# Performance work log

Measured on AMD Instinct MI355X. Metric: run time of the kernel, lower is better.

Reference implementation:

```python
import jax, jax.numpy as jnp
import numpy as np

B, N, E = 256, 128, 262144
LABEL_DIM, MAX_DEGREE, RW_DIM = 29, 16, 16
F = 128
NUM_LABELS = LABEL_DIM + MAX_DEGREE + RW_DIM  # 61
SK_ITER, SK_TAU = 6, 1.0


def _edges(k):
    k1, k2, k3 = jax.random.split(k, 3)
    g = jax.random.randint(k1, (E,), 0, B)
    src = g * N + jax.random.randint(k2, (E,), 0, N)
    dst = g * N + jax.random.randint(k3, (E,), 0, N)
    return src, dst


def setup_inputs():
    key = jax.random.key(0)
    ks = jax.random.split(key, 20)
    ntot = B * N
    s = 0.05
    nrm = lambda k, shp: jax.random.normal(k, shp, dtype=jnp.float32) * s
    src1, dst1 = _edges(ks[3])
    src2, dst2 = _edges(ks[7])
    return {
        'x1': jax.random.uniform(ks[0], (ntot, LABEL_DIM), dtype=jnp.float32),
        'cent1': jax.random.randint(ks[1], (ntot,), 0, MAX_DEGREE),
        'rw1': jax.random.uniform(ks[2], (ntot, RW_DIM), dtype=jnp.float32),
        'src1': src1, 'dst1': dst1,
        'x2': jax.random.uniform(ks[4], (ntot, LABEL_DIM), dtype=jnp.float32),
        'cent2': jax.random.randint(ks[5], (ntot,), 0, MAX_DEGREE),
        'rw2': jax.random.uniform(ks[6], (ntot, RW_DIM), dtype=jnp.float32),
        'src2': src2, 'dst2': dst2,
        'degree_emb': nrm(ks[8], (MAX_DEGREE, MAX_DEGREE)),
        'init_W': nrm(ks[9], (NUM_LABELS, F)), 'init_b': jnp.zeros((F,), jnp.float32),
        'W1': nrm(ks[10], (F, F)), 'b1': jnp.zeros((F,), jnp.float32),
        'W2': nrm(ks[11], (F, F)), 'b2': jnp.zeros((F,), jnp.float32),
        'W3': nrm(ks[12], (F, F)), 'b3': jnp.zeros((F,), jnp.float32),
        'A_aff': nrm(ks[13], (F, F)) + jnp.eye(F, dtype=jnp.float32),
        'sc_W1': nrm(ks[14], (8 * F, 64)), 'sc_b1': jnp.zeros((64,), jnp.float32),
        'sc_W2': nrm(ks[15], (64, 1)), 'sc_b2': jnp.zeros((1,), jnp.float32),
        'topk': 8,
    }


def gcn_conv(x, W, b, src, dst):
    # GCNConv: x' = D^{-1/2} (A + I) D^{-1/2} x W + b
    n = x.shape[0]
    h = x @ W
    loops = jnp.arange(n)
    s = jnp.concatenate([src, loops])
    d = jnp.concatenate([dst, loops])
    deg = jax.ops.segment_sum(jnp.ones_like(d, dtype=h.dtype), d, n)
    dinv = jax.lax.rsqrt(jnp.maximum(deg, 1.0))
    w = dinv[s] * dinv[d]
    return jax.ops.segment_sum(h[s] * w[:, None], d, n) + b


def conv_pass(feat, src, dst, W1, b1, W2, b2, W3, b3):
    f1 = gcn_conv(feat, W1, b1, src, dst)
    f2 = gcn_conv(jax.nn.relu(f1), W2, b2, src, dst)
    f3 = gcn_conv(jax.nn.relu(f2), W3, b3, src, dst)
    return f1, f2, f3


def affinity(xa, xb, A):
    Xa = xa.reshape(B, N, -1)
    Xb = xb.reshape(B, N, -1)
    return jnp.einsum('bif,fg,bjg->bij', Xa, A, Xb)


def soft_topk(scores, ks_tgt, n_iter, tau):
    # Entropic-OT soft top-k (Xie et al.) over flattened affinity entries vs 2 anchors,
    # normalized by SK_ITER log-domain Sinkhorn iterations.
    b, n, m = scores.shape
    L = n * m
    x = scores.reshape(b, L)
    a_lo = x.min(axis=1, keepdims=True) - 1.0
    a_hi = x.max(axis=1, keepdims=True) + 1.0
    anchors = jnp.concatenate([a_lo, a_hi], axis=1)      # [b, 2]
    logK = -jnp.abs(x[:, :, None] - anchors[:, None, :]) / tau  # [b, L, 2]
    log_mu = jnp.full((b, L), -jnp.log(float(L)), dtype=x.dtype)
    k = ks_tgt[:, None]
    nu = jnp.concatenate([(L - k) / L, k / L], axis=1)   # [b, 2]
    log_nu = jnp.log(nu)

    def body(carry, _):
        f, g = carry
        f = log_mu - jax.nn.logsumexp(logK + g[:, None, :], axis=2)
        g = log_nu - jax.nn.logsumexp(logK + f[:, :, None], axis=1)
        return (f, g), None

    init = (jnp.zeros((b, L), x.dtype), jnp.zeros((b, 2), x.dtype))
    (f, g), _ = jax.lax.scan(body, init, None, length=n_iter)
    gamma = jnp.exp(logK + f[:, :, None] + g[:, None, :])
    prob = (gamma[:, :, 1] * L).reshape(b, n, m)
    return gamma, prob


def reference(x1, cent1, rw1, src1, dst1, x2, cent2, rw2, src2, dst2,
              degree_emb, init_W, init_b, W1, b1, W2, b2, W3, b3, A_aff,
              sc_W1, sc_b1, sc_W2, sc_b2, topk):
    feat1 = jax.nn.relu(jnp.concatenate([x1, degree_emb[cent1], rw1], axis=1) @ init_W + init_b)
    feat2 = jax.nn.relu(jnp.concatenate([x2, degree_emb[cent2], rw2], axis=1) @ init_W + init_b)
    f11, f12, f13 = conv_pass(feat1, src1, dst1, W1, b1, W2, b2, W3, b3)
    f21, f22, f23 = conv_pass(feat2, src2, dst2, W1, b1, W2, b2, W3, b3)

    gt_ks = jnp.full((B,), topk / 2.0, dtype=feat1.dtype)
    _, sim1 = soft_topk(affinity(feat1, feat2, A_aff), gt_ks, SK_ITER, SK_TAU)
    _, sim2 = soft_topk(affinity(f13, f23, A_aff), gt_ks, SK_ITER, SK_TAU)

    gf1 = jnp.concatenate([feat1, f11, f12, f13], axis=1).reshape(B, N, -1).sum(axis=1)   # global_add_pool
    gf2 = jnp.concatenate([feat2, f21, f22, f23], axis=1).reshape(B, N, -1).max(axis=1)   # global_max_pool
    scores = jnp.concatenate([gf1, gf2], axis=1)  # [B, 8F]
    h = jax.nn.relu(scores @ sc_W1 + sc_b1)
    ged = jax.nn.sigmoid((h @ sc_W2 + sc_b2).reshape(-1))
    return ged, sim1, sim2
```

## Files before the change

### kernel.cpp

```cpp
#include <hip/hip_runtime.h>
#include <math.h>

#define BATCH 256
#define NNODE 128
#define NT    32768
#define FDIM  128
#define NEDGE 262144
#define LBL   29
#define MAXDEG 16
#define RWD   16
#define NTF   (NT * FDIM)
#define ESTRIDE 2048

__global__ void k_deg2(const int* __restrict__ dst1, const int* __restrict__ dst2,
                       int* __restrict__ d1, int* __restrict__ d2) {
  int e = blockIdx.x * 256 + threadIdx.x;
  if (e < NEDGE) atomicAdd(&d1[dst1[e]], 1);
  else if (e < 2 * NEDGE) atomicAdd(&d2[dst2[e - NEDGE]], 1);
}
__global__ __launch_bounds__(128) void k_scanl(const int* __restrict__ degi1,
                                               int* __restrict__ ofs1, int* __restrict__ cur1,
                                               float* __restrict__ dinv1,
                                               const int* __restrict__ degi2,
                                               int* __restrict__ ofs2, int* __restrict__ cur2,
                                               float* __restrict__ dinv2) {
  const int side = blockIdx.x >> 8;
  const int g = blockIdx.x & 255;
  const int* degi = side ? degi2 : degi1;
  int* ofs   = side ? ofs2  : ofs1;
  int* cur   = side ? cur2  : cur1;
  float* dnv = side ? dinv2 : dinv1;
  const int t = threadIdx.x;
  const int node = g * NNODE + t;
  int dg = degi[node];
  dnv[node] = rsqrtf((float)(dg + 1));
  int lane = t & 63, wv = t >> 6;
  int v = dg;
  for (int off = 1; off < 64; off <<= 1) {
    int u = __shfl_up(v, off);
    if (lane >= off) v += u;
  }
  __shared__ int wsum[2];
  if (lane == 63) wsum[wv] = v;
  __syncthreads();
  int excl = v - dg + (wv ? wsum[0] : 0);
  int base = g * ESTRIDE + excl;
  ofs[node] = base;
  cur[node] = base;
}
__global__ void k_fill2(const int* __restrict__ src1, const int* __restrict__ dst1,
                        int* __restrict__ cur1, int* __restrict__ csr1,
                        const int* __restrict__ src2, const int* __restrict__ dst2,
                        int* __restrict__ cur2, int* __restrict__ csr2) {
  int e = blockIdx.x * 256 + threadIdx.x;
  if (e < NEDGE) {
    int pos = atomicAdd(&cur1[dst1[e]], 1);
    csr1[pos] = src1[e];
  } else if (e < 2 * NEDGE) {
    e -= NEDGE;
    int pos = atomicAdd(&cur2[dst2[e]], 1);
    csr2[pos] = src2[e];
  }
}

__global__ __launch_bounds__(256, 2) void k_chain(
    const float* __restrict__ x1, const int* __restrict__ cent1, const float* __restrict__ rw1,
    const float* __restrict__ x2, const int* __restrict__ cent2, const float* __restrict__ rw2,
    const float* __restrict__ demb,
    const float* __restrict__ initW, const float* __restrict__ initb,
    const float* __restrict__ W1, const float* __restrict__ b1,
    const float* __restrict__ W2, const float* __restrict__ b2,
    const float* __restrict__ W3, const float* __restrict__ b3,
    const int* __restrict__ ofs1, const int* __restrict__ end1, const int* __restrict__ csr1,
    const int* __restrict__ ofs2, const int* __restrict__ end2, const int* __restrict__ csr2,
    const float* __restrict__ dinv1, const float* __restrict__ dinv2,
    float* __restrict__ feat1G, float* __restrict__ feat2G,
    float* __restrict__ f13G, float* __restrict__ f23G,
    float* __restrict__ gfs) {
  __shared__ float X[128 * 132];
  __shared__ float WcB[16 * 132];
  __shared__ float dvL[128];
  __shared__ float bL[128];
  __shared__ int   oL[128], enL[128];

  const int t = threadIdx.x;
  const int side = blockIdx.x >> 8;
  const int g = blockIdx.x & 255;
  const int nb = g * NNODE;

  const float* xg    = side ? x2 : x1;
  const int*   centg = side ? cent2 : cent1;
  const float* rwg   = side ? rw2 : rw1;
  const int*   ofsg  = side ? ofs2 : ofs1;
  const int*   endg  = side ? end2 : end1;
  const int*   csrg  = side ? csr2 : csr1;
  const float* dinvg = side ? dinv2 : dinv1;
  float* featG = side ? feat2G : feat1G;
  float* f3G   = side ? f23G : f13G;

  const int e_base = ofsg[nb];
  if (t < 128) {
    dvL[t] = dinvg[nb + t];
    oL[t]  = ofsg[nb + t] - e_base;
    enL[t] = endg[nb + t] - e_base;
  }
  {
    int d = t >> 1, sub = t & 1;
    int node = nb + d;
    int ct = centg[node];
    const float* xr = xg + (size_t)node * LBL;
    const float* er = demb + ct * MAXDEG;
    const float* rr = rwg + (size_t)node * RWD;
    for (int c = sub * 34; c < sub * 34 + 34; ++c) {
      float v = 0.f;
      if (c < LBL) v = xr[c];
      else if (c < LBL + MAXDEG) v = er[c - LBL];
      else if (c < 61) v = rr[c - 45];
      X[d * 68 + c] = v;
    }
  }
  __syncthreads();

  const int rg = t >> 3;
  const int jq = (t & 7) * 4;

  {
    float acc[4][16] = {};
    for (int kc = 0; kc < 64; kc += 16) {
      __syncthreads();
#pragma unroll
      for (int u = 0; u < 2; ++u) {
        int ll = t + 256 * u;
        int row = ll >> 5, c4 = (ll & 31) * 4;
        int gk = kc + row;
        float4 w = (gk < 61) ? *reinterpret_cast<const float4*>(&initW[(size_t)gk * FDIM + c4])
                             : make_float4(0.f, 0.f, 0.f, 0.f);
        *reinterpret_cast<float4*>(&WcB[row * 132 + c4]) = w;
      }
      if (kc == 0 && t < 128) bL[t] = initb[t];
      __syncthreads();
      for (int kk = 0; kk < 16; kk += 4) {
        float av[4][4];
#pragma unroll
        for (int r = 0; r < 4; ++r) {
          float4 tmp = *reinterpret_cast<const float4*>(&X[(rg + 32 * r) * 68 + kc + kk]);
          av[r][0] = tmp.x; av[r][1] = tmp.y; av[r][2] = tmp.z; av[r][3] = tmp.w;
        }
#pragma unroll
        for (int c = 0; c < 4; ++c) {
          float4 w0 = *reinterpret_cast<const float4*>(&WcB[(kk + c) * 132 + jq]);
          float4 w1 = *reinterpret_cast<const float4*>(&WcB[(kk + c) * 132 + 32 + jq]);
          float4 w2 = *reinterpret_cast<const float4*>(&WcB[(kk + c) * 132 + 64 + jq]);
          float4 w3 = *reinterpret_cast<const float4*>(&WcB[(kk + c) * 132 + 96 + jq]);
#pragma unroll
          for (int r = 0; r < 4; ++r) {
            float a = av[r][c];
            acc[r][0]  += a * w0.x; acc[r][1]  += a * w0.y; acc[r][2]  += a * w0.z; acc[r][3]  += a * w0.w;
            acc[r][4]  += a * w1.x; acc[r][5]  += a * w1.y; acc[r][6]  += a * w1.z; acc[r][7]  += a * w1.w;
            acc[r][8]  += a * w2.x; acc[r][9]  += a * w2.y; acc[r][10] += a * w2.z; acc[r][11] += a * w2.w;
            acc[r][12] += a * w3.x; acc[r][13] += a * w3.y; acc[r][14] += a * w3.z; acc[r][15] += a * w3.w;
          }
        }
      }
    }
    __syncthreads();
#pragma unroll
    for (int r = 0; r < 4; ++r) {
      int row = rg + 32 * r;
#pragma unroll
      for (int q = 0; q < 4; ++q) {
        int col = q * 32 + jq;
        float4 bl = *reinterpret_cast<const float4*>(&bL[col]);
        float4 o = make_float4(fmaxf(acc[r][q * 4 + 0] + bl.x, 0.f),
                               fmaxf(acc[r][q * 4 + 1] + bl.y, 0.f),
                               fmaxf(acc[r][q * 4 + 2] + bl.z, 0.f),
                               fmaxf(acc[r][q * 4 + 3] + bl.w, 0.f));
        *reinterpret_cast<float4*>(&X[row * 132 + col]) = o;
        *reinterpret_cast<float4*>(&featG[(size_t)(nb + row) * FDIM + col]) = o;
      }
    }
    __syncthreads();
  }

#define POOL_LAYER(layer)                                                            \
  {                                                                                  \
    int j4 = (t & 31) * 4, qq = t >> 5;                                              \
    float4 pv = side ? make_float4(-INFINITY, -INFINITY, -INFINITY, -INFINITY)       \
                     : make_float4(0.f, 0.f, 0.f, 0.f);                              \
    for (int r = 0; r < 16; ++r) {                                                   \
      float4 fv = *reinterpret_cast<const float4*>(&X[(qq * 16 + r) * 132 + j4]);    \
      if (side) { pv.x = fmaxf(pv.x, fv.x); pv.y = fmaxf(pv.y, fv.y);                \
                  pv.z = fmaxf(pv.z, fv.z); pv.w = fmaxf(pv.w, fv.w); }              \
      else      { pv.x += fv.x; pv.y += fv.y; pv.z += fv.z; pv.w += fv.w; }          \
    }                                                                                \
    *reinterpret_cast<float4*>(&WcB[qq * 128 + j4]) = pv;                            \
    __syncthreads();                                                                 \
    if (t < 128) {                                                                   \
      float v = side ? -INFINITY : 0.f;                                              \
      for (int q2 = 0; q2 < 8; ++q2) {                                               \
        float w2 = WcB[q2 * 128 + t];                                                \
        v = side ? fmaxf(v, w2) : (v + w2);                                          \
      }                                                                              \
      gfs[g * 1024 + side * 512 + (layer) * 128 + t] = v;                            \
    }                                                                                \
  }

  POOL_LAYER(0)

  for (int l = 0; l < 3; ++l) {
    const float* Wg = (l == 0) ? W1 : (l == 1) ? W2 : W3;
    const float* bg = (l == 0) ? b1 : (l == 1) ? b2 : b3;
    float acc[4][16] = {};
    for (int kc = 0; kc < 128; kc += 16) {
      __syncthreads();
#pragma unroll
      for (int u = 0; u < 2; ++u) {
        int ll = t + 256 * u;
        int row = ll >> 5, c4 = (ll & 31) * 4;
        *reinterpret_cast<float4*>(&WcB[row * 132 + c4]) =
            *reinterpret_cast<const float4*>(&Wg[(size_t)(kc + row) * FDIM + c4]);
      }
      if (kc == 0 && t < 128) bL[t] = bg[t];
      __syncthreads();
      for (int kk = 0; kk < 16; kk += 4) {
        float av[4][4];
#pragma unroll
        for (int r = 0; r < 4; ++r) {
          float4 tmp = *reinterpret_cast<const float4*>(&X[(rg + 32 * r) * 132 + kc + kk]);
          if (l > 0) {
            tmp.x = fmaxf(tmp.x, 0.f); tmp.y = fmaxf(tmp.y, 0.f);
            tmp.z = fmaxf(tmp.z, 0.f); tmp.w = fmaxf(tmp.w, 0.f);
          }
          av[r][0] = tmp.x; av[r][1] = tmp.y; av[r][2] = tmp.z; av[r][3] = tmp.w;
        }
#pragma unroll
        for (int c = 0; c < 4; ++c) {
          float4 w0 = *reinterpret_cast<const float4*>(&WcB[(kk + c) * 132 + jq]);
          float4 w1 = *reinterpret_cast<const float4*>(&WcB[(kk + c) * 132 + 32 + jq]);
          float4 w2 = *reinterpret_cast<const float4*>(&WcB[(kk + c) * 132 + 64 + jq]);
          float4 w3 = *reinterpret_cast<const float4*>(&WcB[(kk + c) * 132 + 96 + jq]);
#pragma unroll
          for (int r = 0; r < 4; ++r) {
            float a = av[r][c];
            acc[r][0]  += a * w0.x; acc[r][1]  += a * w0.y; acc[r][2]  += a * w0.z; acc[r][3]  += a * w0.w;
            acc[r][4]  += a * w1.x; acc[r][5]  += a * w1.y; acc[r][6]  += a * w1.z; acc[r][7]  += a * w1.w;
            acc[r][8]  += a * w2.x; acc[r][9]  += a * w2.y; acc[r][10] += a * w2.z; acc[r][11] += a * w2.w;
            acc[r][12] += a * w3.x; acc[r][13] += a * w3.y; acc[r][14] += a * w3.z; acc[r][15] += a * w3.w;
          }
        }
      }
    }
    __syncthreads();
#pragma unroll
    for (int r = 0; r < 4; ++r) {
      int row = rg + 32 * r;
#pragma unroll
      for (int q = 0; q < 4; ++q) {
        int col = q * 32 + jq;
        *reinterpret_cast<float4*>(&X[row * 132 + col]) =
            make_float4(acc[r][q * 4 + 0], acc[r][q * 4 + 1],
                        acc[r][q * 4 + 2], acc[r][q * 4 + 3]);
      }
    }
    __syncthreads();

    {
      int d = t >> 1, fc = (t & 1) * 64;
      float dd = dvL[d];
      float4 a[16];
#pragma unroll
      for (int u = 0; u < 16; ++u) {
        float4 hv = *reinterpret_cast<const float4*>(&X[d * 132 + fc + u * 4]);
        a[u] = make_float4(dd * hv.x, dd * hv.y, dd * hv.z, dd * hv.w);
      }
      int o0 = oL[d], o1 = enL[d];
      int sj = (o0 < o1) ? (csrg[e_base + o0] - nb) : 0;
      for (int j = o0; j < o1; ++j) {
        int sn = (j + 1 < o1) ? (csrg[e_base + j + 1] - nb) : 0;
        float w = dvL[sj];
#pragma unroll
        for (int u = 0; u < 16; ++u) {
          float4 hv = *reinterpret_cast<const float4*>(&X[sj * 132 + fc + u * 4]);
          a[u].x += w * hv.x; a[u].y += w * hv.y; a[u].z += w * hv.z; a[u].w += w * hv.w;
        }
        sj = sn;
      }
      __syncthreads();
#pragma unroll
      for (int u = 0; u < 16; ++u) {
        float4 bl = *reinterpret_cast<const float4*>(&bL[fc + u * 4]);
        float4 o = make_float4(bl.x + dd * a[u].x, bl.y + dd * a[u].y,
                               bl.z + dd * a[u].z, bl.w + dd * a[u].w);
        *reinterpret_cast<float4*>(&X[d * 132 + fc + u * 4]) = o;
        if (l == 2)
          *reinterpret_cast<float4*>(&f3G[(size_t)(nb + d) * FDIM + fc + u * 4]) = o;
      }
    }
    __syncthreads();

    POOL_LAYER(l + 1)
  }
#undef POOL_LAYER
}

__global__ __launch_bounds__(1024) void k_sim(const float* __restrict__ F1s1,
                                              const float* __restrict__ F2s1,
                                              const float* __restrict__ F1s2,
                                              const float* __restrict__ F2s2,
                                              const float* __restrict__ Aaff,
                                              const int* __restrict__ topk,
                                              float* __restrict__ S1,
                                              float* __restrict__ S2) {
  __shared__ float X1[128 * 132];
  __shared__ float X2[128 * 132];
  __shared__ float rA[16], rB[16], bc[2];

  const int t = threadIdx.x;
  const int half = blockIdx.x >> 8;
  const int b = blockIdx.x & 255;
  const float* F1b = (half ? F1s2 : F1s1) + (size_t)b * NNODE * FDIM;
  const float* F2b = (half ? F2s2 : F2s1) + (size_t)b * NNODE * FDIM;
  float* Sout = (half ? S2 : S1) + (size_t)b * NNODE * NNODE;

#pragma unroll
  for (int p = 0; p < 4; ++p) {
    int fi = t + 1024 * p;
    int row = fi >> 5, c4 = (fi & 31) * 4;
    *reinterpret_cast<float4*>(&X1[row * 132 + c4]) =
        *reinterpret_cast<const float4*>(&Aaff[(size_t)row * FDIM + c4]);
  }
  {
    int row = t >> 3;
    int cq  = (t & 7) * 4;
#pragma unroll
    for (int p = 0; p < 4; ++p) {
      int c4 = p * 32 + cq;
      float4 v = *reinterpret_cast<const float4*>(&F2b[(size_t)row * FDIM + c4]);
      X2[(c4 + 0) * 132 + row] = v.x;
      X2[(c4 + 1) * 132 + row] = v.y;
      X2[(c4 + 2) * 132 + row] = v.z;
      X2[(c4 + 3) * 132 + row] = v.w;
    }
  }
  __syncthreads();

  const int rw = t >> 4;
  const int jq4 = (t & 15) * 4;
  const float* f1r0 = F1b + (size_t)rw * FDIM;
  const float* f1r1 = F1b + (size_t)(rw + 64) * FDIM;

  float acc[2][8] = {};

  for (int k0 = 0; k0 < 128; k0 += 4) {
    float4 a40 = *reinterpret_cast<const float4*>(&f1r0[k0]);
    float4 a41 = *reinterpret_cast<const float4*>(&f1r1[k0]);
    float av0[4] = {a40.x, a40.y, a40.z, a40.w};
    float av1[4] = {a41.x, a41.y, a41.z, a41.w};
#pragma unroll
    for (int c = 0; c < 4; ++c) {
      const float* wb = &X1[(k0 + c) * 132];
      float4 w0 = *reinterpret_cast<const float4*>(&wb[jq4]);
      float4 w1 = *reinterpret_cast<const float4*>(&wb[jq4 + 64]);
      float a0 = av0[c], a1 = av1[c];
      acc[0][0] += a0 * w0.x; acc[0][1] += a0 * w0.y; acc[0][2] += a0 * w0.z; acc[0][3] += a0 * w0.w;
      acc[0][4] += a0 * w1.x; acc[0][5] += a0 * w1.y; acc[0][6] += a0 * w1.z; acc[0][7] += a0 * w1.w;
      acc[1][0] += a1 * w0.x; acc[1][1] += a1 * w0.y; acc[1][2] += a1 * w0.z; acc[1][3] += a1 * w0.w;
      acc[1][4] += a1 * w1.x; acc[1][5] += a1 * w1.y; acc[1][6] += a1 * w1.z; acc[1][7] += a1 * w1.w;
    }
  }
  __syncthreads();
  *reinterpret_cast<float4*>(&X1[rw * 132 + jq4]) =
      make_float4(acc[0][0], acc[0][1], acc[0][2], acc[0][3]);
  *reinterpret_cast<float4*>(&X1[rw * 132 + jq4 + 64]) =
      make_float4(acc[0][4], acc[0][5], acc[0][6], acc[0][7]);
  *reinterpret_cast<float4*>(&X1[(rw + 64) * 132 + jq4]) =
      make_float4(acc[1][0], acc[1][1], acc[1][2], acc[1][3]);
  *reinterpret_cast<float4*>(&X1[(rw + 64) * 132 + jq4 + 64]) =
      make_float4(acc[1][4], acc[1][5], acc[1][6], acc[1][7]);

#pragma unroll
  for (int r = 0; r < 2; ++r)
#pragma unroll
    for (int j = 0; j < 8; ++j) acc[r][j] = 0.f;
  __syncthreads();

  for (int k0 = 0; k0 < 128; k0 += 4) {
    float4 a40 = *reinterpret_cast<const float4*>(&X1[rw * 132 + k0]);
    float4 a41 = *reinterpret_cast<const float4*>(&X1[(rw + 64) * 132 + k0]);
    float av0[4] = {a40.x, a40.y, a40.z, a40.w};
    float av1[4] = {a41.x, a41.y, a41.z, a41.w};
#pragma unroll
    for (int c = 0; c < 4; ++c) {
      const float* wb = &X2[(k0 + c) * 132];
      float4 w0 = *reinterpret_cast<const float4*>(&wb[jq4]);
      float4 w1 = *reinterpret_cast<const float4*>(&wb[jq4 + 64]);
      float a0 = av0[c], a1 = av1[c];
      acc[0][0] += a0 * w0.x; acc[0][1] += a0 * w0.y; acc[0][2] += a0 * w0.z; acc[0][3] += a0 * w0.w;
      acc[0][4] += a0 * w1.x; acc[0][5] += a0 * w1.y; acc[0][6] += a0 * w1.z; acc[0][7] += a0 * w1.w;
      acc[1][0] += a1 * w0.x; acc[1][1] += a1 * w0.y; acc[1][2] += a1 * w0.z; acc[1][3] += a1 * w0.w;
      acc[1][4] += a1 * w1.x; acc[1][5] += a1 * w1.y; acc[1][6] += a1 * w1.z; acc[1][7] += a1 * w1.w;
    }
  }

  const float* af = &acc[0][0];
  const int wave = t >> 6, lane = t & 63;
  {
    float mn = af[0], mx = af[0];
#pragma unroll
    for (int u = 1; u < 16; ++u) { mn = fminf(mn, af[u]); mx = fmaxf(mx, af[u]); }
    for (int off = 32; off; off >>= 1) {
      mn = fminf(mn, __shfl_down(mn, off));
      mx = fmaxf(mx, __shfl_down(mx, off));
    }
    if (lane == 0) { rA[wave] = mn; rB[wave] = mx; }
    __syncthreads();
    if (t < 16) {
      mn = rA[t]; mx = rB[t];
      for (int off = 8; off; off >>= 1) {
        mn = fminf(mn, __shfl_down(mn, off));
        mx = fmaxf(mx, __shfl_down(mx, off));
      }
      if (t == 0) { bc[0] = mn - 1.f; bc[1] = mx + 1.f; }
    }
    __syncthreads();
  }
  float a_lo = bc[0], a_hi = bc[1];

  float p[16], q[16];
#pragma unroll
  for (int u = 0; u < 16; ++u) {
    p[u] = __expf(a_lo - af[u]);
    q[u] = __expf(af[u] - a_hi);
  }

  const float Lf = (float)(NNODE * NNODE);
  float kt = 0.5f * (float)topk[0];

  float E0 = 1.f, E1 = 1.f, E0p = 1.f, E1p = 1.f;
  for (int it = 0; it < 6; ++it) {
    E0p = E0; E1p = E1;
    float r0 = 0.f, r1 = 0.f;
#pragma unroll
    for (int u = 0; u < 16; ++u) {
      float denom = fmaf(p[u], E0, q[u] * E1);
      float rin = __builtin_amdgcn_rcpf(denom);
      r0 = fmaf(p[u], rin, r0);
      r1 = fmaf(q[u], rin, r1);
    }
    for (int off = 32; off; off >>= 1) {
      r0 += __shfl_down(r0, off);
      r1 += __shfl_down(r1, off);
    }
    if (lane == 0) { rA[wave] = r0; rB[wave] = r1; }
    __syncthreads();
    if (t < 16) {
      r0 = rA[t]; r1 = rB[t];
      for (int off = 8; off; off >>= 1) {
        r0 += __shfl_down(r0, off);
        r1 += __shfl_down(r1, off);
      }
      if (t == 0) { bc[0] = (Lf - kt) / r0; bc[1] = kt / r1; }
    }
    __syncthreads();
    E0 = bc[0]; E1 = bc[1];
    __syncthreads();
  }

#pragma unroll
  for (int r = 0; r < 2; ++r) {
    float* xrow = Sout + (size_t)(rw + r * 64) * NNODE;
#pragma unroll
    for (int qd = 0; qd < 2; ++qd) {
      float o[4];
#pragma unroll
      for (int j = 0; j < 4; ++j) {
        int u = r * 8 + qd * 4 + j;
        float denom = fmaf(p[u], E0p, q[u] * E1p);
        o[j] = q[u] * E1 * __builtin_amdgcn_rcpf(denom);
      }
      *reinterpret_cast<float4*>(&xrow[jq4 + qd * 64]) = make_float4(o[0], o[1], o[2], o[3]);
    }
  }
}

__global__ __launch_bounds__(256) void k_mlp(const float* __restrict__ gfs,
                                             const float* __restrict__ W1,
                                             const float* __restrict__ b1,
                                             const float* __restrict__ W2,
                                             const float* __restrict__ b2,
                                             float* __restrict__ ged) {
  __shared__ float sm[1024];
  int b = blockIdx.x, t = threadIdx.x;
  const float* s = gfs + b * 1024;
#pragma unroll
  for (int qq = 0; qq < 4; ++qq) sm[t + 256 * qq] = s[t + 256 * qq];
  __syncthreads();
  int j4 = (t & 15) * 4, kp = t >> 4;
  float4 acc = make_float4(0.f, 0.f, 0.f, 0.f);
#pragma unroll 8
  for (int k = 0; k < 64; ++k) {
    float4 w = *reinterpret_cast<const float4*>(&W1[(size_t)(kp * 64 + k) * 64 + j4]);
    float sv = sm[kp * 64 + k];
    acc.x += sv * w.x; acc.y += sv * w.y; acc.z += sv * w.z; acc.w += sv * w.w;
  }
  __syncthreads();
  *reinterpret_cast<float4*>(&sm[kp * 64 + j4]) = acc;
  __syncthreads();
  if (t < 64) {
    float h = b1[t];
#pragma unroll
    for (int kp2 = 0; kp2 < 16; ++kp2) h += sm[kp2 * 64 + t];
    h = fmaxf(h, 0.f);
    float v = h * W2[t];
    for (int off = 32; off; off >>= 1) v += __shfl_down(v, off);
    if (t == 0) ged[b] = 1.f / (1.f + __expf(-(v + b2[0])));
  }
}

extern "C" void kernel_launch(void* const* d_in, const int* in_sizes, int n_in,
                              void* d_out, int out_size, void* d_ws, size_t ws_size,
                              hipStream_t stream) {
  (void)in_sizes; (void)n_in; (void)out_size; (void)ws_size;
  const float* x1    = (const float*)d_in[0];
  const int*   cent1 = (const int*)  d_in[1];
  const float* rw1   = (const float*)d_in[2];
  const int*   src1  = (const int*)  d_in[3];
  const int*   dst1  = (const int*)  d_in[4];
  const float* x2    = (const float*)d_in[5];
  const int*   cent2 = (const int*)  d_in[6];
  const float* rw2   = (const float*)d_in[7];
  const int*   src2  = (const int*)  d_in[8];
  const int*   dst2  = (const int*)  d_in[9];
  const float* demb  = (const float*)d_in[10];
  const float* initW = (const float*)d_in[11];
  const float* initb = (const float*)d_in[12];
  const float* W1    = (const float*)d_in[13];
  const float* b1    = (const float*)d_in[14];
  const float* W2    = (const float*)d_in[15];
  const float* b2    = (const float*)d_in[16];
  const float* W3    = (const float*)d_in[17];
  const float* b3    = (const float*)d_in[18];
  const float* Aaff  = (const float*)d_in[19];
  const float* scW1  = (const float*)d_in[20];
  const float* scb1  = (const float*)d_in[21];
  const float* scW2  = (const float*)d_in[22];
  const float* scb2  = (const float*)d_in[23];
  const int*   topk  = (const int*)  d_in[24];

  float* ws    = (float*)d_ws;
  float* feat1 = ws;
  float* feat2 = ws + (size_t)1 * NTF;
  float* f13   = ws + (size_t)2 * NTF;
  float* f23   = ws + (size_t)3 * NTF;
  float* dinv1 = ws + (size_t)4 * NTF;
  float* dinv2 = dinv1 + NT;
  float* gfs   = dinv2 + NT;

  float* ged = (float*)d_out;
  float* S1  = ged + BATCH;
  float* S2  = S1 + (size_t)BATCH * NNODE * NNODE;

  int* degi1 = (int*)S1;
  int* ofs1  = degi1 + NT;
  int* cur1  = ofs1 + NT;
  int* csr1  = cur1 + NT;
  int* degi2 = csr1 + BATCH * ESTRIDE;
  int* ofs2  = degi2 + NT;
  int* cur2  = ofs2 + NT;
  int* csr2  = ofs2 + 2 * NT;

  const int gE = NEDGE / 256;

  hipMemsetAsync(degi1, 0, NT * sizeof(int), stream);
  hipMemsetAsync(degi2, 0, NT * sizeof(int), stream);
  k_deg2<<<2 * gE, 256, 0, stream>>>(dst1, dst2, degi1, degi2);
  k_scanl<<<512, 128, 0, stream>>>(degi1, ofs1, cur1, dinv1, degi2, ofs2, cur2, dinv2);
  k_fill2<<<2 * gE, 256, 0, stream>>>(src1, dst1, cur1, csr1, src2, dst2, cur2, csr2);

  k_chain<<<512, 256, 0, stream>>>(
      x1, cent1, rw1, x2, cent2, rw2, demb, initW, initb,
      W1, b1, W2, b2, W3, b3,
      ofs1, cur1, csr1, ofs2, cur2, csr2, dinv1, dinv2,
      feat1, feat2, f13, f23, gfs);

  k_mlp<<<BATCH, 256, 0, stream>>>(gfs, scW1, scb1, scW2, scb2, ged);

  k_sim<<<512, 1024, 0, stream>>>(feat1, feat2, f13, f23, Aaff, topk, S1, S2);
}
```

Baseline: 413.9 us.

## Replace CSR degree-scan build with fixed-slot per-node adjacency lists

New measurement: 391.3 us. -5.5%, faster.

```diff
diff --git a/kernel.cpp b/kernel.cpp
--- a/kernel.cpp
+++ b/kernel.cpp
@@ -10,56 +10,22 @@
 #define MAXDEG 16
 #define RWD   16
 #define NTF   (NT * FDIM)
-#define ESTRIDE 2048
-
-__global__ void k_deg2(const int* __restrict__ dst1, const int* __restrict__ dst2,
-                       int* __restrict__ d1, int* __restrict__ d2) {
-  int e = blockIdx.x * 256 + threadIdx.x;
-  if (e < NEDGE) atomicAdd(&d1[dst1[e]], 1);
-  else if (e < 2 * NEDGE) atomicAdd(&d2[dst2[e - NEDGE]], 1);
-}
-__global__ __launch_bounds__(128) void k_scanl(const int* __restrict__ degi1,
-                                               int* __restrict__ ofs1, int* __restrict__ cur1,
-                                               float* __restrict__ dinv1,
-                                               const int* __restrict__ degi2,
-                                               int* __restrict__ ofs2, int* __restrict__ cur2,
-                                               float* __restrict__ dinv2) {
-  const int side = blockIdx.x >> 8;
-  const int g = blockIdx.x & 255;
-  const int* degi = side ? degi2 : degi1;
-  int* ofs   = side ? ofs2  : ofs1;
-  int* cur   = side ? cur2  : cur1;
-  float* dnv = side ? dinv2 : dinv1;
-  const int t = threadIdx.x;
-  const int node = g * NNODE + t;
-  int dg = degi[node];
-  dnv[node] = rsqrtf((float)(dg + 1));
-  int lane = t & 63, wv = t >> 6;
-  int v = dg;
-  for (int off = 1; off < 64; off <<= 1) {
-    int u = __shfl_up(v, off);
-    if (lane >= off) v += u;
-  }
-  __shared__ int wsum[2];
-  if (lane == 63) wsum[wv] = v;
-  __syncthreads();
-  int excl = v - dg + (wv ? wsum[0] : 0);
-  int base = g * ESTRIDE + excl;
-  ofs[node] = base;
-  cur[node] = base;
-}
-__global__ void k_fill2(const int* __restrict__ src1, const int* __restrict__ dst1,
-                        int* __restrict__ cur1, int* __restrict__ csr1,
-                        const int* __restrict__ src2, const int* __restrict__ dst2,
-                        int* __restrict__ cur2, int* __restrict__ csr2) {
+#define DSLOT 64
+
+__global__ void k_fill(const int* __restrict__ src1, const int* __restrict__ dst1,
+                       int* __restrict__ cnt1, int* __restrict__ csr1,
+                       const int* __restrict__ src2, const int* __restrict__ dst2,
+                       int* __restrict__ cnt2, int* __restrict__ csr2) {
   int e = blockIdx.x * 256 + threadIdx.x;
   if (e < NEDGE) {
-    int pos = atomicAdd(&cur1[dst1[e]], 1);
-    csr1[pos] = src1[e];
+    int node = dst1[e];
+    int pos = atomicAdd(&cnt1[node], 1);
+    csr1[(size_t)node * DSLOT + pos] = src1[e];
   } else if (e < 2 * NEDGE) {
     e -= NEDGE;
-    int pos = atomicAdd(&cur2[dst2[e]], 1);
-    csr2[pos] = src2[e];
+    int node = dst2[e];
+    int pos = atomicAdd(&cnt2[node], 1);
+    csr2[(size_t)node * DSLOT + pos] = src2[e];
   }
 }
 
@@ -71,9 +37,8 @@
     const float* __restrict__ W1, const float* __restrict__ b1,
     const float* __restrict__ W2, const float* __restrict__ b2,
     const float* __restrict__ W3, const float* __restrict__ b3,
-    const int* __restrict__ ofs1, const int* __restrict__ end1, const int* __restrict__ csr1,
-    const int* __restrict__ ofs2, const int* __restrict__ end2, const int* __restrict__ csr2,
-    const float* __restrict__ dinv1, const float* __restrict__ dinv2,
+    const int* __restrict__ cnt1, const int* __restrict__ csr1,
+    const int* __restrict__ cnt2, const int* __restrict__ csr2,
     float* __restrict__ feat1G, float* __restrict__ feat2G,
     float* __restrict__ f13G, float* __restrict__ f23G,
     float* __restrict__ gfs) {
@@ -81,7 +46,7 @@
   __shared__ float WcB[16 * 132];
   __shared__ float dvL[128];
   __shared__ float bL[128];
-  __shared__ int   oL[128], enL[128];
+  __shared__ int   cnL[128];
 
   const int t = threadIdx.x;
   const int side = blockIdx.x >> 8;
@@ -91,18 +56,15 @@
   const float* xg    = side ? x2 : x1;
   const int*   centg = side ? cent2 : cent1;
   const float* rwg   = side ? rw2 : rw1;
-  const int*   ofsg  = side ? ofs2 : ofs1;
-  const int*   endg  = side ? end2 : end1;
+  const int*   cntg  = side ? cnt2 : cnt1;
   const int*   csrg  = side ? csr2 : csr1;
-  const float* dinvg = side ? dinv2 : dinv1;
   float* featG = side ? feat2G : feat1G;
   float* f3G   = side ? f23G : f13G;
 
-  const int e_base = ofsg[nb];
   if (t < 128) {
-    dvL[t] = dinvg[nb + t];
-    oL[t]  = ofsg[nb + t] - e_base;
-    enL[t] = endg[nb + t] - e_base;
+    int dg = cntg[nb + t];
+    dvL[t] = rsqrtf((float)(dg + 1));
+    cnL[t] = dg;
   }
   {
     int d = t >> 1, sub = t & 1;
@@ -273,10 +235,11 @@
         float4 hv = *reinterpret_cast<const float4*>(&X[d * 132 + fc + u * 4]);
         a[u] = make_float4(dd * hv.x, dd * hv.y, dd * hv.z, dd * hv.w);
       }
-      int o0 = oL[d], o1 = enL[d];
-      int sj = (o0 < o1) ? (csrg[e_base + o0] - nb) : 0;
-      for (int j = o0; j < o1; ++j) {
-        int sn = (j + 1 < o1) ? (csrg[e_base + j + 1] - nb) : 0;
+      const int* elist = csrg + (size_t)(nb + d) * DSLOT;
+      int cntd = cnL[d];
+      int sj = (cntd > 0) ? (elist[0] - nb) : 0;
+      for (int j = 0; j < cntd; ++j) {
+        int sn = (j + 1 < cntd) ? (elist[j + 1] - nb) : 0;
         float w = dvL[sj];
 #pragma unroll
         for (int u = 0; u < 16; ++u) {
@@ -552,35 +515,27 @@
   float* feat2 = ws + (size_t)1 * NTF;
   float* f13   = ws + (size_t)2 * NTF;
   float* f23   = ws + (size_t)3 * NTF;
-  float* dinv1 = ws + (size_t)4 * NTF;
-  float* dinv2 = dinv1 + NT;
-  float* gfs   = dinv2 + NT;
+  float* gfs   = ws + (size_t)4 * NTF;
 
   float* ged = (float*)d_out;
   float* S1  = ged + BATCH;
   float* S2  = S1 + (size_t)BATCH * NNODE * NNODE;
 
-  int* degi1 = (int*)S1;
-  int* ofs1  = degi1 + NT;
-  int* cur1  = ofs1 + NT;
-  int* csr1  = cur1 + NT;
-  int* degi2 = csr1 + BATCH * ESTRIDE;
-  int* ofs2  = degi2 + NT;
-  int* cur2  = ofs2 + NT;
-  int* csr2  = ofs2 + 2 * NT;
+  int* cnt1 = (int*)S1;
+  int* csr1 = cnt1 + NT;
+  int* cnt2 = (int*)S2;
+  int* csr2 = cnt2 + NT;
 
   const int gE = NEDGE / 256;
 
-  hipMemsetAsync(degi1, 0, NT * sizeof(int), stream);
-  hipMemsetAsync(degi2, 0, NT * sizeof(int), stream);
-  k_deg2<<<2 * gE, 256, 0, stream>>>(dst1, dst2, degi1, degi2);
-  k_scanl<<<512, 128, 0, stream>>>(degi1, ofs1, cur1, dinv1, degi2, ofs2, cur2, dinv2);
-  k_fill2<<<2 * gE, 256, 0, stream>>>(src1, dst1, cur1, csr1, src2, dst2, cur2, csr2);
+  hipMemsetAsync(cnt1, 0, NT * sizeof(int), stream);
+  hipMemsetAsync(cnt2, 0, NT * sizeof(int), stream);
+  k_fill<<<2 * gE, 256, 0, stream>>>(src1, dst1, cnt1, csr1, src2, dst2, cnt2, csr2);
 
   k_chain<<<512, 256, 0, stream>>>(
       x1, cent1, rw1, x2, cent2, rw2, demb, initW, initb,
       W1, b1, W2, b2, W3, b3,
-      ofs1, cur1, csr1, ofs2, cur2, csr2, dinv1, dinv2,
+      cnt1, csr1, cnt2, csr2,
       feat1, feat2, f13, f23, gfs);
 
   k_mlp<<<BATCH, 256, 0, stream>>>(gfs, scW1, scb1, scW2, scb2, ged);
```
